# Optimization experiments

Measured on AMD Instinct MI355X. Metric: run time of the kernel, lower is better.

## Reference

```python
import jax, jax.numpy as jnp
import numpy as np


def _ternary(x, delta):
    # {-1, 0, +1} thresholded at +/- delta
    return jnp.where(x > delta, 1.0, jnp.where(x < -delta, -1.0, 0.0)).astype(x.dtype)


def setup_inputs() -> dict:
    key = jax.random.key(0)
    kx, kw = jax.random.split(key)
    x = jax.random.normal(kx, (8192, 4096), dtype=jnp.float32)
    weight = jax.random.normal(kw, (4096, 4096), dtype=jnp.float32) * 0.02
    return {"x": x, "weight": weight}


def reference(x, weight):
    # TernaryActivation: delta = 0.1 * mean|x|
    x_q = _ternary(x, 0.1 * jnp.mean(jnp.abs(x)))
    # TernaryQuantize: delta = 0.05 * mean|w|, scaled by alpha = mean|w|
    w_abs_mean = jnp.mean(jnp.abs(weight))
    w_q = w_abs_mean * _ternary(weight, 0.05 * w_abs_mean)
    # F.linear(x_q, w_q) = x_q @ w_q.T
    return jnp.einsum('bi,oi->bo', x_q, w_q)
```

## Files before the change

### kernel.cpp

```cpp
#include <hip/hip_runtime.h>
#include <stdint.h>

typedef __attribute__((ext_vector_type(4))) int i32x4;
typedef __attribute__((ext_vector_type(16))) float f32x16;

#define MROWS 8192L
#define NCOLS 4096L
#define KDIM  4096L

#define XQ_BYTES   (MROWS * KDIM / 2)
#define WQ_BYTES   (NCOLS * KDIM / 2)
#define SCAL_OFF   (XQ_BYTES + WQ_BYTES)

__global__ __launch_bounds__(256) void k_reduce_abs(const float* __restrict__ x,
                                                    const float* __restrict__ w,
                                                    float* __restrict__ partials) {
    __shared__ float sm[256];
    int b = blockIdx.x;
    int t = threadIdx.x;
    const float4* v;
    long base;
    if (b < 512) { v = (const float4*)x; base = (long)b * 16384; }
    else         { v = (const float4*)w; base = (long)(b - 512) * 16384; }
    float s = 0.f;
    for (int i = t; i < 16384; i += 256) {
        float4 q = v[base + i];
        s += fabsf(q.x) + fabsf(q.y) + fabsf(q.z) + fabsf(q.w);
    }
    sm[t] = s;
    __syncthreads();
    for (int off = 128; off > 0; off >>= 1) {
        if (t < off) sm[t] += sm[t + off];
        __syncthreads();
    }
    if (t == 0) partials[b] = sm[0];
}

__global__ __launch_bounds__(256) void k_finalize(float* __restrict__ scal) {
    const float* partials = scal + 4;
    __shared__ double sm[256];
    int t = threadIdx.x;

    double sx = 0.0;
    for (int i = t; i < 512; i += 256) sx += (double)partials[i];
    sm[t] = sx;
    __syncthreads();
    for (int off = 128; off > 0; off >>= 1) {
        if (t < off) sm[t] += sm[t + off];
        __syncthreads();
    }
    double SX = sm[0];
    __syncthreads();

    double sw = (double)partials[512 + t];
    sm[t] = sw;
    __syncthreads();
    for (int off = 128; off > 0; off >>= 1) {
        if (t < off) sm[t] += sm[t + off];
        __syncthreads();
    }
    if (t == 0) {
        float meanx = (float)(SX / 33554432.0);
        float meanw = (float)(sm[0] / 16777216.0);
        scal[0] = 0.1f * meanx;
        scal[1] = 0.05f * meanw;
        scal[2] = meanw;
    }
}

__device__ __forceinline__ unsigned int nib4(float v, float delta) {
    return v > delta ? 2u : (v < -delta ? 10u : 0u);
}

__global__ __launch_bounds__(256) void k_quantF(const float* __restrict__ x,
                                                const float* __restrict__ w,
                                                uint4* __restrict__ xq,
                                                uint4* __restrict__ wq,
                                                const float* __restrict__ scal) {
    int wv = blockIdx.x * 4 + (threadIdx.x >> 6);
    int l = threadIdx.x & 63;

    const float* src;
    uint4* dst;
    float delta;
    int task;
    if (wv < 16384) {
        src = x; dst = xq; delta = scal[0]; task = wv;
    } else {
        src = w; dst = wq; delta = scal[1]; task = wv - 16384;
    }
    int rowblk = task >> 6;
    int rest = task & 63;
    long row = (long)rowblk * 32 + (l & 31);
    long fidx = row * 4096 + (long)(rest >> 1) * 128 + (long)(rest & 1) * 64
              + (long)(l >> 5) * 32;
    const float4* s4 = (const float4*)(src + fidx);

    unsigned int ow[4];
#pragma unroll
    for (int c = 0; c < 4; ++c) {
        float4 q0 = s4[2 * c];
        float4 q1 = s4[2 * c + 1];
        ow[c] = nib4(q0.x, delta)
              | (nib4(q0.y, delta) << 4)
              | (nib4(q0.z, delta) << 8)
              | (nib4(q0.w, delta) << 12)
              | (nib4(q1.x, delta) << 16)
              | (nib4(q1.y, delta) << 20)
              | (nib4(q1.z, delta) << 24)
              | (nib4(q1.w, delta) << 28);
    }
    uint4 o; o.x = ow[0]; o.y = ow[1]; o.z = ow[2]; o.w = ow[3];
    dst[(long)task * 64 + l] = o;
}

#define GLOAD_LDS16(g, l)                                                             \
    __builtin_amdgcn_global_load_lds((const __attribute__((address_space(1))) void*)(g), \
                                     (__attribute__((address_space(3))) void*)(l),       \
                                     16, 0, 0)

#define MK8(v) __builtin_shufflevector((v), (v), 0, 1, 2, 3, -1, -1, -1, -1)

#define MFMA32(a, b, c)                                                       \
    __builtin_amdgcn_mfma_scale_f32_32x32x64_f8f6f4(MK8(a), MK8(b), (c),      \
        4, 4, 0, 0x7F7F7F7F, 0, 0x7F7F7F7F)

__global__ __launch_bounds__(512, 2) void k_gemm(const signed char* __restrict__ Xq,
                                                 const signed char* __restrict__ Wq,
                                                 float* __restrict__ out,
                                                 const float* __restrict__ scal) {
    __shared__ __attribute__((aligned(16))) signed char lds[131072];

    const float alpha = scal[2];

    int bid = (int)blockIdx.x;
    bid = (bid & 7) * 64 + (bid >> 3);
    int bm = bid >> 4;
    int bn = bid & 15;
    long row0 = (long)bm * 256;
    long col0 = (long)bn * 256;

    int t = threadIdx.x;
    int lane = t & 63;
    int wid = t >> 6;
    int wm = wid >> 2;
    int wn = wid & 3;

    const signed char* sp[4];
    int ldoff[4];
#pragma unroll
    for (int j = 0; j < 4; ++j) {
        int g = wid * 4 + j;
        ldoff[j] = g * 1024;
        if (g < 16) {
            long rowblk = bm * 8 + (g >> 3) * 4 + ((g >> 1) & 3);
            sp[j] = Xq + rowblk * 65536 + (g & 1) * 1024 + lane * 16;
        } else {
            int h = g - 16;
            long colblk = bn * 8 + (h >> 2) * 2 + ((h >> 1) & 1);
            sp[j] = Wq + colblk * 65536 + (h & 1) * 1024 + lane * 16;
        }
    }

#define STAGE(slot, g1) do {                                                   \
    signed char* sb_ = lds + (slot) * 32768;                                   \
    _Pragma("unroll")                                                          \
    for (int j_ = 0; j_ < 4; ++j_)                                             \
        GLOAD_LDS16(sp[j_] + (long)(g1) * 2048, sb_ + ldoff[j_]);              \
} while (0)

    const signed char* Ab = lds + wm * 8192 + lane * 16;
    const signed char* Bb = lds + 16384 + wn * 4096 + lane * 16;

    f32x16 acc[4][2];
#pragma unroll
    for (int i = 0; i < 4; ++i)
#pragma unroll
        for (int j = 0; j < 2; ++j)
            acc[i][j] = (f32x16){0.f};

    STAGE(0, 0);
    STAGE(1, 1);
    STAGE(2, 2);

    for (int g = 0; g < 32; ++g) {
        int slot = g & 3;
        __builtin_amdgcn_s_barrier();
        if (g < 29) {
            STAGE((g + 3) & 3, g + 3);
            asm volatile("s_waitcnt vmcnt(12)" ::: "memory");
        } else if (g == 29) {
            asm volatile("s_waitcnt vmcnt(8)" ::: "memory");
        } else if (g == 30) {
            asm volatile("s_waitcnt vmcnt(4)" ::: "memory");
        } else {
            asm volatile("s_waitcnt vmcnt(0)" ::: "memory");
        }
        __builtin_amdgcn_s_barrier();
        __builtin_amdgcn_sched_barrier(0);

        const signed char* A = Ab + slot * 32768;
        const signed char* B = Bb + slot * 32768;

        i32x4 a00, a01, a10, a11, a20, a21, a30, a31;
        i32x4 b00, b01, b10, b11;
        b00 = *(const i32x4*)(B + 0 * 1024);
        b01 = *(const i32x4*)(B + 1 * 1024);
        b10 = *(const i32x4*)(B + 2 * 1024);
        b11 = *(const i32x4*)(B + 3 * 1024);
        a00 = *(const i32x4*)(A + 0 * 1024);
        a01 = *(const i32x4*)(A + 1 * 1024);
        a10 = *(const i32x4*)(A + 2 * 1024);
        a11 = *(const i32x4*)(A + 3 * 1024);
        __builtin_amdgcn_s_setprio(1);
        acc[0][0] = MFMA32(a00, b00, acc[0][0]);
        acc[0][1] = MFMA32(a00, b10, acc[0][1]);
        acc[1][0] = MFMA32(a10, b00, acc[1][0]);
        acc[1][1] = MFMA32(a10, b10, acc[1][1]);
        acc[0][0] = MFMA32(a01, b01, acc[0][0]);
        acc[0][1] = MFMA32(a01, b11, acc[0][1]);
        acc[1][0] = MFMA32(a11, b01, acc[1][0]);
        acc[1][1] = MFMA32(a11, b11, acc[1][1]);
        __builtin_amdgcn_s_setprio(0);
        a20 = *(const i32x4*)(A + 4 * 1024);
        a21 = *(const i32x4*)(A + 5 * 1024);
        a30 = *(const i32x4*)(A + 6 * 1024);
        a31 = *(const i32x4*)(A + 7 * 1024);
        __builtin_amdgcn_s_setprio(1);
        acc[2][0] = MFMA32(a20, b00, acc[2][0]);
        acc[2][1] = MFMA32(a20, b10, acc[2][1]);
        acc[3][0] = MFMA32(a30, b00, acc[3][0]);
        acc[3][1] = MFMA32(a30, b10, acc[3][1]);
        acc[2][0] = MFMA32(a21, b01, acc[2][0]);
        acc[2][1] = MFMA32(a21, b11, acc[2][1]);
        acc[3][0] = MFMA32(a31, b01, acc[3][0]);
        acc[3][1] = MFMA32(a31, b11, acc[3][1]);
        __builtin_amdgcn_s_setprio(0);
    }

#pragma unroll
    for (int mi = 0; mi < 4; ++mi) {
#pragma unroll
        for (int ni = 0; ni < 2; ++ni) {
            long col = col0 + wn * 64 + ni * 32 + (lane & 31);
            long rowb = row0 + wm * 128 + mi * 32 + 4 * (lane >> 5);
#pragma unroll
            for (int r = 0; r < 16; ++r) {
                long row = rowb + (r & 3) + 8 * (r >> 2);
                out[row * NCOLS + col] = alpha * acc[mi][ni][r];
            }
        }
    }
#undef STAGE
}

extern "C" void kernel_launch(void* const* d_in, const int* in_sizes, int n_in,
                              void* d_out, int out_size, void* d_ws, size_t ws_size,
                              hipStream_t stream) {
    const float* x = (const float*)d_in[0];
    const float* w = (const float*)d_in[1];
    float* out = (float*)d_out;

    uint8_t* ws = (uint8_t*)d_ws;
    signed char* Xq = (signed char*)ws;
    signed char* Wq = (signed char*)(ws + XQ_BYTES);
    float* scal = (float*)(ws + SCAL_OFF);

    k_reduce_abs<<<768, 256, 0, stream>>>(x, w, scal + 4);
    k_finalize<<<1, 256, 0, stream>>>(scal);
    k_quantF<<<6144, 256, 0, stream>>>(x, w, (uint4*)Xq, (uint4*)Wq, scal);
    k_gemm<<<512, 512, 0, stream>>>(Xq, Wq, out, scal);
}
```

Baseline: 156.3 us.

## Process two K-stages per barrier pair and interleave LDS reads with MFMAs

The GEMM main loop now consumes two 4-slot LDS stages per iteration, issuing two stage prefetches at once. That halves the number of barrier pairs and waitcnt points. The compute body is restructured so LDS fragment loads are interleaved with the MFMAs that consume them, and the s_setprio hints are dropped. The prefetch depth changes from three stages ahead to two ahead issued in pairs, which may expose more memory latency at each double-step.

```diff
diff --git a/kernel.cpp b/kernel.cpp
--- a/kernel.cpp
+++ b/kernel.cpp
@@ -179,63 +179,58 @@
         for (int j = 0; j < 2; ++j)
             acc[i][j] = (f32x16){0.f};
 
+#define BODY(slot) do {                                                        \
+    const signed char* A = Ab + (slot) * 32768;                                \
+    const signed char* B = Bb + (slot) * 32768;                                \
+    i32x4 b00 = *(const i32x4*)(B + 0 * 1024);                                 \
+    i32x4 b10 = *(const i32x4*)(B + 2 * 1024);                                 \
+    i32x4 a00 = *(const i32x4*)(A + 0 * 1024);                                 \
+    i32x4 a10 = *(const i32x4*)(A + 2 * 1024);                                 \
+    acc[0][0] = MFMA32(a00, b00, acc[0][0]);                                   \
+    acc[1][0] = MFMA32(a10, b00, acc[1][0]);                                   \
+    acc[0][1] = MFMA32(a00, b10, acc[0][1]);                                   \
+    acc[1][1] = MFMA32(a10, b10, acc[1][1]);                                   \
+    i32x4 b01 = *(const i32x4*)(B + 1 * 1024);                                 \
+    i32x4 b11 = *(const i32x4*)(B + 3 * 1024);                                 \
+    i32x4 a01 = *(const i32x4*)(A + 1 * 1024);                                 \
+    i32x4 a11 = *(const i32x4*)(A + 3 * 1024);                                 \
+    acc[0][0] = MFMA32(a01, b01, acc[0][0]);                                   \
+    acc[1][0] = MFMA32(a11, b01, acc[1][0]);                                   \
+    acc[0][1] = MFMA32(a01, b11, acc[0][1]);                                   \
+    acc[1][1] = MFMA32(a11, b11, acc[1][1]);                                   \
+    i32x4 a20 = *(const i32x4*)(A + 4 * 1024);                                 \
+    i32x4 a30 = *(const i32x4*)(A + 6 * 1024);                                 \
+    acc[2][0] = MFMA32(a20, b00, acc[2][0]);                                   \
+    acc[3][0] = MFMA32(a30, b00, acc[3][0]);                                   \
+    acc[2][1] = MFMA32(a20, b10, acc[2][1]);                                   \
+    acc[3][1] = MFMA32(a30, b10, acc[3][1]);                                   \
+    i32x4 a21 = *(const i32x4*)(A + 5 * 1024);                                 \
+    i32x4 a31 = *(const i32x4*)(A + 7 * 1024);                                 \
+    acc[2][0] = MFMA32(a21, b01, acc[2][0]);                                   \
+    acc[3][0] = MFMA32(a31, b01, acc[3][0]);                                   \
+    acc[2][1] = MFMA32(a21, b11, acc[2][1]);                                   \
+    acc[3][1] = MFMA32(a31, b11, acc[3][1]);                                   \
+} while (0)
+
     STAGE(0, 0);
     STAGE(1, 1);
-    STAGE(2, 2);
-
-    for (int g = 0; g < 32; ++g) {
-        int slot = g & 3;
+
+    for (int d = 0; d < 16; ++d) {
+        int s0 = (2 * d) & 3;
+        int s1 = (2 * d + 1) & 3;
         __builtin_amdgcn_s_barrier();
-        if (g < 29) {
-            STAGE((g + 3) & 3, g + 3);
-            asm volatile("s_waitcnt vmcnt(12)" ::: "memory");
-        } else if (g == 29) {
+        if (d < 15) {
+            STAGE((2 * d + 2) & 3, 2 * d + 2);
+            STAGE((2 * d + 3) & 3, 2 * d + 3);
             asm volatile("s_waitcnt vmcnt(8)" ::: "memory");
-        } else if (g == 30) {
-            asm volatile("s_waitcnt vmcnt(4)" ::: "memory");
         } else {
             asm volatile("s_waitcnt vmcnt(0)" ::: "memory");
         }
         __builtin_amdgcn_s_barrier();
         __builtin_amdgcn_sched_barrier(0);
 
-        const signed char* A = Ab + slot * 32768;
-        const signed char* B = Bb + slot * 32768;
-
-        i32x4 a00, a01, a10, a11, a20, a21, a30, a31;
-        i32x4 b00, b01, b10, b11;
-        b00 = *(const i32x4*)(B + 0 * 1024);
-        b01 = *(const i32x4*)(B + 1 * 1024);
-        b10 = *(const i32x4*)(B + 2 * 1024);
-        b11 = *(const i32x4*)(B + 3 * 1024);
-        a00 = *(const i32x4*)(A + 0 * 1024);
-        a01 = *(const i32x4*)(A + 1 * 1024);
-        a10 = *(const i32x4*)(A + 2 * 1024);
-        a11 = *(const i32x4*)(A + 3 * 1024);
-        __builtin_amdgcn_s_setprio(1);
-        acc[0][0] = MFMA32(a00, b00, acc[0][0]);
-        acc[0][1] = MFMA32(a00, b10, acc[0][1]);
-        acc[1][0] = MFMA32(a10, b00, acc[1][0]);
-        acc[1][1] = MFMA32(a10, b10, acc[1][1]);
-        acc[0][0] = MFMA32(a01, b01, acc[0][0]);
-        acc[0][1] = MFMA32(a01, b11, acc[0][1]);
-        acc[1][0] = MFMA32(a11, b01, acc[1][0]);
-        acc[1][1] = MFMA32(a11, b11, acc[1][1]);
-        __builtin_amdgcn_s_setprio(0);
-        a20 = *(const i32x4*)(A + 4 * 1024);
-        a21 = *(const i32x4*)(A + 5 * 1024);
-        a30 = *(const i32x4*)(A + 6 * 1024);
-        a31 = *(const i32x4*)(A + 7 * 1024);
-        __builtin_amdgcn_s_setprio(1);
-        acc[2][0] = MFMA32(a20, b00, acc[2][0]);
-        acc[2][1] = MFMA32(a20, b10, acc[2][1]);
-        acc[3][0] = MFMA32(a30, b00, acc[3][0]);
-        acc[3][1] = MFMA32(a30, b10, acc[3][1]);
-        acc[2][0] = MFMA32(a21, b01, acc[2][0]);
-        acc[2][1] = MFMA32(a21, b11, acc[2][1]);
-        acc[3][0] = MFMA32(a31, b01, acc[3][0]);
-        acc[3][1] = MFMA32(a31, b11, acc[3][1]);
-        __builtin_amdgcn_s_setprio(0);
+        BODY(s0);
+        BODY(s1);
     }
 
 #pragma unroll
@@ -251,6 +246,7 @@
             }
         }
     }
+#undef BODY
 #undef STAGE
 }
 
```

After: 153.8 us. No clear change (-1.7%).

## Load GEMM operands directly from global into registers, dropping LDS staging

Applied to the files above, without the earlier changes.

Replaces the 4-slot LDS ring buffer (global_load_lds plus barriers) with direct per-wave global loads into registers, software-pipelined one k-step ahead and interleaved with the MFMAs. This removes LDS traffic, the two block barriers per iteration and the 128 KB shared allocation, which could raise occupancy. The cost is that tiles are no longer shared across waves: each wave refetches its A/B fragments from global/L2, raising cache bandwidth demand, and only one step of prefetch may not hide global latency.

```diff
diff --git a/kernel.cpp b/kernel.cpp
--- a/kernel.cpp
+++ b/kernel.cpp
@@ -114,11 +114,6 @@
     dst[(long)task * 64 + l] = o;
 }
 
-#define GLOAD_LDS16(g, l)                                                             \
-    __builtin_amdgcn_global_load_lds((const __attribute__((address_space(1))) void*)(g), \
-                                     (__attribute__((address_space(3))) void*)(l),       \
-                                     16, 0, 0)
-
 #define MK8(v) __builtin_shufflevector((v), (v), 0, 1, 2, 3, -1, -1, -1, -1)
 
 #define MFMA32(a, b, c)                                                       \
@@ -129,8 +124,6 @@
                                                  const signed char* __restrict__ Wq,
                                                  float* __restrict__ out,
                                                  const float* __restrict__ scal) {
-    __shared__ __attribute__((aligned(16))) signed char lds[131072];
-
     const float alpha = scal[2];
 
     int bid = (int)blockIdx.x;
@@ -146,31 +139,20 @@
     int wm = wid >> 2;
     int wn = wid & 3;
 
-    const signed char* sp[4];
-    int ldoff[4];
-#pragma unroll
-    for (int j = 0; j < 4; ++j) {
-        int g = wid * 4 + j;
-        ldoff[j] = g * 1024;
-        if (g < 16) {
-            long rowblk = bm * 8 + (g >> 3) * 4 + ((g >> 1) & 3);
-            sp[j] = Xq + rowblk * 65536 + (g & 1) * 1024 + lane * 16;
-        } else {
-            int h = g - 16;
-            long colblk = bn * 8 + (h >> 2) * 2 + ((h >> 1) & 1);
-            sp[j] = Wq + colblk * 65536 + (h & 1) * 1024 + lane * 16;
-        }
-    }
-
-#define STAGE(slot, g1) do {                                                   \
-    signed char* sb_ = lds + (slot) * 32768;                                   \
-    _Pragma("unroll")                                                          \
-    for (int j_ = 0; j_ < 4; ++j_)                                             \
-        GLOAD_LDS16(sp[j_] + (long)(g1) * 2048, sb_ + ldoff[j_]);              \
-} while (0)
-
-    const signed char* Ab = lds + wm * 8192 + lane * 16;
-    const signed char* Bb = lds + 16384 + wn * 4096 + lane * 16;
+    const signed char* pa[4][2];
+    const signed char* pb[2][2];
+#pragma unroll
+    for (int mi = 0; mi < 4; ++mi)
+#pragma unroll
+        for (int ks = 0; ks < 2; ++ks)
+            pa[mi][ks] = Xq + (long)(bm * 8 + wm * 4 + mi) * 65536 + ks * 1024 + lane * 16;
+#pragma unroll
+    for (int ni = 0; ni < 2; ++ni)
+#pragma unroll
+        for (int ks = 0; ks < 2; ++ks)
+            pb[ni][ks] = Wq + (long)(bn * 8 + wn * 2 + ni) * 65536 + ks * 1024 + lane * 16;
+
+#define LD(p, off) (*(const i32x4*)((p) + (off)))
 
     f32x16 acc[4][2];
 #pragma unroll
@@ -179,63 +161,44 @@
         for (int j = 0; j < 2; ++j)
             acc[i][j] = (f32x16){0.f};
 
-    STAGE(0, 0);
-    STAGE(1, 1);
-    STAGE(2, 2);
+    i32x4 a00 = LD(pa[0][0], 0), a10 = LD(pa[1][0], 0);
+    i32x4 a20 = LD(pa[2][0], 0), a30 = LD(pa[3][0], 0);
+    i32x4 b00 = LD(pb[0][0], 0), b10 = LD(pb[1][0], 0);
+    i32x4 a01 = LD(pa[0][1], 0), a11 = LD(pa[1][1], 0);
+    i32x4 a21 = LD(pa[2][1], 0), a31 = LD(pa[3][1], 0);
+    i32x4 b01 = LD(pb[0][1], 0), b11 = LD(pb[1][1], 0);
 
     for (int g = 0; g < 32; ++g) {
-        int slot = g & 3;
-        __builtin_amdgcn_s_barrier();
-        if (g < 29) {
-            STAGE((g + 3) & 3, g + 3);
-            asm volatile("s_waitcnt vmcnt(12)" ::: "memory");
-        } else if (g == 29) {
-            asm volatile("s_waitcnt vmcnt(8)" ::: "memory");
-        } else if (g == 30) {
-            asm volatile("s_waitcnt vmcnt(4)" ::: "memory");
-        } else {
-            asm volatile("s_waitcnt vmcnt(0)" ::: "memory");
-        }
-        __builtin_amdgcn_s_barrier();
-        __builtin_amdgcn_sched_barrier(0);
-
-        const signed char* A = Ab + slot * 32768;
-        const signed char* B = Bb + slot * 32768;
-
-        i32x4 a00, a01, a10, a11, a20, a21, a30, a31;
-        i32x4 b00, b01, b10, b11;
-        b00 = *(const i32x4*)(B + 0 * 1024);
-        b01 = *(const i32x4*)(B + 1 * 1024);
-        b10 = *(const i32x4*)(B + 2 * 1024);
-        b11 = *(const i32x4*)(B + 3 * 1024);
-        a00 = *(const i32x4*)(A + 0 * 1024);
-        a01 = *(const i32x4*)(A + 1 * 1024);
-        a10 = *(const i32x4*)(A + 2 * 1024);
-        a11 = *(const i32x4*)(A + 3 * 1024);
-        __builtin_amdgcn_s_setprio(1);
+        long kn = (long)((g + 1) & 31) * 2048;
+
         acc[0][0] = MFMA32(a00, b00, acc[0][0]);
+        acc[1][0] = MFMA32(a10, b00, acc[1][0]);
         acc[0][1] = MFMA32(a00, b10, acc[0][1]);
-        acc[1][0] = MFMA32(a10, b00, acc[1][0]);
         acc[1][1] = MFMA32(a10, b10, acc[1][1]);
+        a00 = LD(pa[0][0], kn);
+        a10 = LD(pa[1][0], kn);
+        acc[2][0] = MFMA32(a20, b00, acc[2][0]);
+        acc[3][0] = MFMA32(a30, b00, acc[3][0]);
+        acc[2][1] = MFMA32(a20, b10, acc[2][1]);
+        acc[3][1] = MFMA32(a30, b10, acc[3][1]);
+        a20 = LD(pa[2][0], kn);
+        a30 = LD(pa[3][0], kn);
+        b00 = LD(pb[0][0], kn);
+        b10 = LD(pb[1][0], kn);
         acc[0][0] = MFMA32(a01, b01, acc[0][0]);
+        acc[1][0] = MFMA32(a11, b01, acc[1][0]);
         acc[0][1] = MFMA32(a01, b11, acc[0][1]);
-        acc[1][0] = MFMA32(a11, b01, acc[1][0]);
         acc[1][1] = MFMA32(a11, b11, acc[1][1]);
-        __builtin_amdgcn_s_setprio(0);
-        a20 = *(const i32x4*)(A + 4 * 1024);
-        a21 = *(const i32x4*)(A + 5 * 1024);
-        a30 = *(const i32x4*)(A + 6 * 1024);
-        a31 = *(const i32x4*)(A + 7 * 1024);
-        __builtin_amdgcn_s_setprio(1);
-        acc[2][0] = MFMA32(a20, b00, acc[2][0]);
-        acc[2][1] = MFMA32(a20, b10, acc[2][1]);
-        acc[3][0] = MFMA32(a30, b00, acc[3][0]);
-        acc[3][1] = MFMA32(a30, b10, acc[3][1]);
+        a01 = LD(pa[0][1], kn);
+        a11 = LD(pa[1][1], kn);
         acc[2][0] = MFMA32(a21, b01, acc[2][0]);
+        acc[3][0] = MFMA32(a31, b01, acc[3][0]);
         acc[2][1] = MFMA32(a21, b11, acc[2][1]);
-        acc[3][0] = MFMA32(a31, b01, acc[3][0]);
         acc[3][1] = MFMA32(a31, b11, acc[3][1]);
-        __builtin_amdgcn_s_setprio(0);
+        a21 = LD(pa[2][1], kn);
+        a31 = LD(pa[3][1], kn);
+        b01 = LD(pb[0][1], kn);
+        b11 = LD(pb[1][1], kn);
     }
 
 #pragma unroll
@@ -251,7 +214,7 @@
             }
         }
     }
-#undef STAGE
+#undef LD
 }
 
 extern "C" void kernel_launch(void* const* d_in, const int* in_sizes, int n_in,
```

Result: slower. 184.8 us (+18.2%).

## Shrink GEMM tile to 256x128 with double buffering for higher occupancy

Applied to the files above, without the earlier changes.

The GEMM block tile shrinks from 256x256 to 256x128, and the launch doubles to 1024 blocks. The 4-stage LDS pipeline (128 KB) becomes a 2-stage double buffer (48 KB), which lets up to four blocks share a CU. Each wave now holds a 2x2 grid of MFMA accumulators instead of 4x2, with its A/B LDS loads interleaved between MFMA groups. The aim is more waves in flight to hide latency, at the cost of less data reuse per block, more global traffic, and a shallower prefetch.

```diff
diff --git a/kernel.cpp b/kernel.cpp
--- a/kernel.cpp
+++ b/kernel.cpp
@@ -125,125 +125,106 @@
     __builtin_amdgcn_mfma_scale_f32_32x32x64_f8f6f4(MK8(a), MK8(b), (c),      \
         4, 4, 0, 0x7F7F7F7F, 0, 0x7F7F7F7F)
 
-__global__ __launch_bounds__(512, 2) void k_gemm(const signed char* __restrict__ Xq,
+__global__ __launch_bounds__(512, 4) void k_gemm(const signed char* __restrict__ Xq,
                                                  const signed char* __restrict__ Wq,
                                                  float* __restrict__ out,
                                                  const float* __restrict__ scal) {
-    __shared__ __attribute__((aligned(16))) signed char lds[131072];
+    __shared__ __attribute__((aligned(16))) signed char lds[49152];
 
     const float alpha = scal[2];
 
     int bid = (int)blockIdx.x;
-    bid = (bid & 7) * 64 + (bid >> 3);
-    int bm = bid >> 4;
-    int bn = bid & 15;
+    bid = (bid & 7) * 128 + (bid >> 3);
+    int bm = bid >> 5;
+    int bn = bid & 31;
     long row0 = (long)bm * 256;
-    long col0 = (long)bn * 256;
+    long col0 = (long)bn * 128;
 
     int t = threadIdx.x;
     int lane = t & 63;
     int wid = t >> 6;
-    int wm = wid >> 2;
-    int wn = wid & 3;
-
-    const signed char* sp[4];
-    int ldoff[4];
-#pragma unroll
-    for (int j = 0; j < 4; ++j) {
-        int g = wid * 4 + j;
+    int wm = wid >> 1;
+    int wn = wid & 1;
+
+    const signed char* sp[3];
+    int ldoff[3];
+#pragma unroll
+    for (int j = 0; j < 3; ++j) {
+        int g = wid * 3 + j;
         ldoff[j] = g * 1024;
         if (g < 16) {
-            long rowblk = bm * 8 + (g >> 3) * 4 + ((g >> 1) & 3);
+            long rowblk = bm * 8 + (g >> 2) * 2 + ((g >> 1) & 1);
             sp[j] = Xq + rowblk * 65536 + (g & 1) * 1024 + lane * 16;
         } else {
             int h = g - 16;
-            long colblk = bn * 8 + (h >> 2) * 2 + ((h >> 1) & 1);
+            long colblk = bn * 4 + (h >> 2) * 2 + ((h >> 1) & 1);
             sp[j] = Wq + colblk * 65536 + (h & 1) * 1024 + lane * 16;
         }
     }
 
 #define STAGE(slot, g1) do {                                                   \
-    signed char* sb_ = lds + (slot) * 32768;                                   \
+    signed char* sb_ = lds + (slot) * 24576;                                   \
     _Pragma("unroll")                                                          \
-    for (int j_ = 0; j_ < 4; ++j_)                                             \
+    for (int j_ = 0; j_ < 3; ++j_)                                             \
         GLOAD_LDS16(sp[j_] + (long)(g1) * 2048, sb_ + ldoff[j_]);              \
 } while (0)
 
-    const signed char* Ab = lds + wm * 8192 + lane * 16;
+    const signed char* Ab = lds + wm * 4096 + lane * 16;
     const signed char* Bb = lds + 16384 + wn * 4096 + lane * 16;
 
-    f32x16 acc[4][2];
-#pragma unroll
-    for (int i = 0; i < 4; ++i)
+    f32x16 acc[2][2];
+#pragma unroll
+    for (int i = 0; i < 2; ++i)
 #pragma unroll
         for (int j = 0; j < 2; ++j)
             acc[i][j] = (f32x16){0.f};
 
     STAGE(0, 0);
-    STAGE(1, 1);
-    STAGE(2, 2);
-
+
+#pragma unroll 2
     for (int g = 0; g < 32; ++g) {
-        int slot = g & 3;
+        int slot = g & 1;
         __builtin_amdgcn_s_barrier();
-        if (g < 29) {
-            STAGE((g + 3) & 3, g + 3);
-            asm volatile("s_waitcnt vmcnt(12)" ::: "memory");
-        } else if (g == 29) {
-            asm volatile("s_waitcnt vmcnt(8)" ::: "memory");
-        } else if (g == 30) {
-            asm volatile("s_waitcnt vmcnt(4)" ::: "memory");
+        if (g < 31) {
+            STAGE(slot ^ 1, g + 1);
+            asm volatile("s_waitcnt vmcnt(3)" ::: "memory");
         } else {
             asm volatile("s_waitcnt vmcnt(0)" ::: "memory");
         }
         __builtin_amdgcn_s_barrier();
         __builtin_amdgcn_sched_barrier(0);
 
-        const signed char* A = Ab + slot * 32768;
-        const signed char* B = Bb + slot * 32768;
-
-        i32x4 a00, a01, a10, a11, a20, a21, a30, a31;
-        i32x4 b00, b01, b10, b11;
-        b00 = *(const i32x4*)(B + 0 * 1024);
-        b01 = *(const i32x4*)(B + 1 * 1024);
-        b10 = *(const i32x4*)(B + 2 * 1024);
-        b11 = *(const i32x4*)(B + 3 * 1024);
-        a00 = *(const i32x4*)(A + 0 * 1024);
-        a01 = *(const i32x4*)(A + 1 * 1024);
-        a10 = *(const i32x4*)(A + 2 * 1024);
-        a11 = *(const i32x4*)(A + 3 * 1024);
+        const signed char* A = Ab + slot * 24576;
+        const signed char* B = Bb + slot * 24576;
+
+        i32x4 a00 = *(const i32x4*)(A + 0 * 1024);
+        i32x4 a10 = *(const i32x4*)(A + 2 * 1024);
+        i32x4 b00 = *(const i32x4*)(B + 0 * 1024);
+        i32x4 b10 = *(const i32x4*)(B + 2 * 1024);
         __builtin_amdgcn_s_setprio(1);
         acc[0][0] = MFMA32(a00, b00, acc[0][0]);
+        acc[1][0] = MFMA32(a10, b00, acc[1][0]);
         acc[0][1] = MFMA32(a00, b10, acc[0][1]);
-        acc[1][0] = MFMA32(a10, b00, acc[1][0]);
         acc[1][1] = MFMA32(a10, b10, acc[1][1]);
+        __builtin_amdgcn_s_setprio(0);
+        i32x4 a01 = *(const i32x4*)(A + 1 * 1024);
+        i32x4 a11 = *(const i32x4*)(A + 3 * 1024);
+        i32x4 b01 = *(const i32x4*)(B + 1 * 1024);
+        i32x4 b11 = *(const i32x4*)(B + 3 * 1024);
+        __builtin_amdgcn_s_setprio(1);
         acc[0][0] = MFMA32(a01, b01, acc[0][0]);
+        acc[1][0] = MFMA32(a11, b01, acc[1][0]);
         acc[0][1] = MFMA32(a01, b11, acc[0][1]);
-        acc[1][0] = MFMA32(a11, b01, acc[1][0]);
         acc[1][1] = MFMA32(a11, b11, acc[1][1]);
         __builtin_amdgcn_s_setprio(0);
-        a20 = *(const i32x4*)(A + 4 * 1024);
-        a21 = *(const i32x4*)(A + 5 * 1024);
-        a30 = *(const i32x4*)(A + 6 * 1024);
-        a31 = *(const i32x4*)(A + 7 * 1024);
-        __builtin_amdgcn_s_setprio(1);
-        acc[2][0] = MFMA32(a20, b00, acc[2][0]);
-        acc[2][1] = MFMA32(a20, b10, acc[2][1]);
-        acc[3][0] = MFMA32(a30, b00, acc[3][0]);
-        acc[3][1] = MFMA32(a30, b10, acc[3][1]);
-        acc[2][0] = MFMA32(a21, b01, acc[2][0]);
-        acc[2][1] = MFMA32(a21, b11, acc[2][1]);
-        acc[3][0] = MFMA32(a31, b01, acc[3][0]);
-        acc[3][1] = MFMA32(a31, b11, acc[3][1]);
-        __builtin_amdgcn_s_setprio(0);
-    }
-
-#pragma unroll
-    for (int mi = 0; mi < 4; ++mi) {
+    }
+
+#pragma unroll
+    for (int mi = 0; mi < 2; ++mi) {
 #pragma unroll
         for (int ni = 0; ni < 2; ++ni) {
             long col = col0 + wn * 64 + ni * 32 + (lane & 31);
-            long rowb = row0 + wm * 128 + mi * 32 + 4 * (lane >> 5);
+            long rowb = row0 + wm * 64 + mi * 32 + 4 * (lane >> 5);
 #pragma unroll
             for (int r = 0; r < 16; ++r) {
                 long row = rowb + (r & 3) + 8 * (r >> 2);
@@ -269,5 +250,5 @@
     k_reduce_abs<<<768, 256, 0, stream>>>(x, w, scal + 4);
     k_finalize<<<1, 256, 0, stream>>>(scal);
     k_quantF<<<6144, 256, 0, stream>>>(x, w, (uint4*)Xq, (uint4*)Wq, scal);
-    k_gemm<<<512, 512, 0, stream>>>(Xq, Wq, out, scal);
-}
+    k_gemm<<<1024, 512, 0, stream>>>(Xq, Wq, out, scal);
+}
```

After: 154.8 us. No clear change (-1.0%).
